# Kernel tuning notes

Hardware: AMD Instinct MI355X
Metric: run time of the kernel (lower is better)

Reference implementation:

```python
import jax, jax.numpy as jnp
import numpy as np

B, IN, OUT, D = 8192, 1024, 1024, 8


def setup_inputs() -> dict:
    key = jax.random.key(0)
    k1, k2, k3, k4 = jax.random.split(key, 4)
    # kaiming-uniform-ish init for weights, uniform for biases (values don't affect correctness)
    bound = 1.0 / np.sqrt(IN)
    return {
        "input": jax.random.normal(k1, (B, IN), dtype=jnp.float32),
        "w": jax.random.uniform(k2, (B, D), dtype=jnp.float32),
        "weights": jax.random.uniform(k3, (D, OUT, IN), dtype=jnp.float32, minval=-bound, maxval=bound),
        "biases": jax.random.uniform(k4, (D, OUT), dtype=jnp.float32, minval=-bound, maxval=bound),
    }


def reference(input, w, weights, biases):
    # Original math: weight[b] = sum_d w[b,d] * weights[d]  (shape [out,in])
    #                out[b]    = input[b] @ weight[b].T + sum_d w[b,d]*biases[d]
    # Restructured as one big GEMM + cheap dsize reduction:
    # tmp[b,d,o] = sum_i input[b,i] * weights[d,o,i]   (GEMM: [B,in] x [in, d*out])
    tmp = jnp.einsum('bi,doi->bdo', input, weights)
    out = jnp.einsum('bdo,bd->bo', tmp, w) + w @ biases
    return out
```

## Files before the change

### kernel.cpp

```cpp
#include <hip/hip_runtime.h>
#include <stdint.h>

typedef unsigned short u16;
typedef float v4f __attribute__((ext_vector_type(4)));
typedef short v8s __attribute__((ext_vector_type(8)));

#define B_   8192
#define IN_  1024
#define OUT_ 1024
#define D_   8

#define BM 128
#define BN 128
#define BK 64

__device__ __forceinline__ u16 f2bf(float f) {
  uint32_t u = __float_as_uint(f);
  u += 0x7fffu + ((u >> 16) & 1u);
  return (u16)(u >> 16);
}

__global__ __launch_bounds__(256) void convert_both(
    const float* __restrict__ input, const float* __restrict__ weights,
    u16* __restrict__ inBf, u16* __restrict__ wtBf) {
  int i4 = blockIdx.x * blockDim.x + threadIdx.x;
  const int n4 = (B_ * IN_) / 4;
  const float* src;
  u16* dst;
  int idx;
  if (i4 < n4) { src = input;   dst = inBf; idx = i4; }
  else         { src = weights; dst = wtBf; idx = i4 - n4; }
  float4 v = ((const float4*)src)[idx];
  ushort4 o;
  o.x = f2bf(v.x); o.y = f2bf(v.y); o.z = f2bf(v.z); o.w = f2bf(v.w);
  ((ushort4*)dst)[idx] = o;
}

__device__ __forceinline__ void gload_lds16(const u16* g, u16* l) {
  typedef __attribute__((address_space(1))) void gvoid;
  typedef __attribute__((address_space(3))) void lvoid;
  __builtin_amdgcn_global_load_lds((gvoid*)g, (lvoid*)l, 16, 0, 0);
}

__global__ __launch_bounds__(256, 2) void gemm_rs(
    const u16* __restrict__ A,
    const u16* __restrict__ Wt,
    const float* __restrict__ w,
    const float* __restrict__ biases,
    float* __restrict__ out) {
  __shared__ __align__(16) u16 As[2][BM * BK];
  __shared__ __align__(16) u16 Bs[3][BN * BK];

  const int id   = blockIdx.x;
  const int xcd  = id & 7;
  const int slot = id >> 3;
  const int by   = xcd + ((slot & 7) << 3);
  const int bx   = slot >> 3;

  const int tid  = threadIdx.x;
  const int wid  = tid >> 6;
  const int lane = tid & 63;
  const int wr   = wid >> 1, wc = wid & 1;
  const int quad = lane >> 4, l16 = lane & 15;
  const int m0   = by * BM;
  const int n0   = bx * BN;

  const int swz  = (lane & 7) ^ ((lane >> 3) & 7);
  const int rowS = wid * 32 + (lane >> 3);
  const u16* aBase[4];
  const u16* bBase[4];
  int cOff[4];
#pragma unroll
  for (int j = 0; j < 4; ++j) {
    const int row = rowS + j * 8;
    aBase[j] = A  + (size_t)(m0 + row) * IN_ + swz * 8;
    bBase[j] = Wt + (size_t)(n0 + row) * IN_ + swz * 8;
    cOff[j]  = (wid * 256 + j * 64 + lane) * 8;
  }

  const int aRow = wr * 64 + l16;
  const int bRow = wc * 64 + l16;
  const int e    = l16 & 7;
  int aCol[2];
#pragma unroll
  for (int h = 0; h < 2; ++h) aCol[h] = ((quad + 4 * h) ^ e) * 8;

  const v4f vzero = {0.f, 0.f, 0.f, 0.f};
  v4f acc[4][4];
#pragma unroll
  for (int mt = 0; mt < 4; ++mt)
#pragma unroll
    for (int nt = 0; nt < 4; ++nt) acc[mt][nt] = vzero;

  float wp[4][4];
#pragma unroll
  for (int mt = 0; mt < 4; ++mt)
#pragma unroll
    for (int r = 0; r < 4; ++r) {
      const int grow = m0 + wr * 64 + mt * 16 + quad * 4 + r;
      wp[mt][r] = fmaxf(w[(size_t)grow * D_], 1e-30f);
    }

  u16* aC_ = As[0];
  u16* aN  = As[1];
  u16* bC  = Bs[0];
  u16* bN  = Bs[1];
  u16* bS  = Bs[2];

#pragma unroll
  for (int j = 0; j < 4; ++j) gload_lds16(aBase[j], aC_ + cOff[j]);
#pragma unroll
  for (int j = 0; j < 4; ++j) gload_lds16(bBase[j], bC + cOff[j]);
#pragma unroll
  for (int j = 0; j < 4; ++j)
    gload_lds16(bBase[j] + (size_t)BK, bN + cOff[j]);
  asm volatile("s_waitcnt vmcnt(4) lgkmcnt(0)" ::: "memory");
  __builtin_amdgcn_s_barrier();

  for (int dd = 0; dd < D_; ++dd) {
    if (dd > 0) {
#pragma unroll
      for (int mt = 0; mt < 4; ++mt) {
#pragma unroll
        for (int r = 0; r < 4; ++r) {
          const int grow = m0 + wr * 64 + mt * 16 + quad * 4 + r;
          const float wn = fmaxf(w[(size_t)grow * D_ + dd], 1e-30f);
          const float ratio = wp[mt][r] / wn;
          wp[mt][r] = wn;
#pragma unroll
          for (int nt = 0; nt < 4; ++nt) acc[mt][nt][r] *= ratio;
        }
      }
    }
    for (int it = 0; it < 16; ++it) {
      const int t = dd * 16 + it;

      if (t < 127) {
        const int sit = (it + 1) & 15;
#pragma unroll
        for (int j = 0; j < 4; ++j)
          gload_lds16(aBase[j] + sit * BK, aN + cOff[j]);
      }
      if (t < 126) {
        const int it2  = it + 2;
        const int sdd2 = dd + (it2 >> 4);
        const int sit2 = it2 & 15;
#pragma unroll
        for (int j = 0; j < 4; ++j)
          gload_lds16(bBase[j] + (size_t)sdd2 * (OUT_ * IN_) + sit2 * BK,
                      bS + cOff[j]);
      }

      __builtin_amdgcn_s_setprio(1);
#pragma unroll
      for (int h = 0; h < 2; ++h) {
        v8s af[4], bf[4];
#pragma unroll
        for (int mt = 0; mt < 4; ++mt)
          af[mt] = *(const v8s*)(aC_ + (aRow + mt * 16) * BK + aCol[h]);
#pragma unroll
        for (int nt = 0; nt < 4; ++nt)
          bf[nt] = *(const v8s*)(bC + (bRow + nt * 16) * BK + aCol[h]);
#pragma unroll
        for (int mt = 0; mt < 4; ++mt)
#pragma unroll
          for (int nt = 0; nt < 4; ++nt)
            acc[mt][nt] = __builtin_amdgcn_mfma_f32_16x16x32_bf16(
                af[mt], bf[nt], acc[mt][nt], 0, 0, 0);
      }
      __builtin_amdgcn_s_setprio(0);

      if (t < 126) {
        asm volatile("s_waitcnt vmcnt(4)" ::: "memory");
        __builtin_amdgcn_s_barrier();
      } else if (t == 126) {
        asm volatile("s_waitcnt vmcnt(0)" ::: "memory");
        __builtin_amdgcn_s_barrier();
      }

      u16* ta = aC_; aC_ = aN; aN = ta;
      u16* tb = bC; bC = bN; bN = bS; bS = tb;
    }
  }

  float bcol[4][8];
#pragma unroll
  for (int nt = 0; nt < 4; ++nt) {
    const int col = n0 + wc * 64 + nt * 16 + l16;
#pragma unroll
    for (int dd = 0; dd < 8; ++dd) bcol[nt][dd] = biases[dd * OUT_ + col];
  }
#pragma unroll
  for (int mt = 0; mt < 4; ++mt) {
#pragma unroll
    for (int r = 0; r < 4; ++r) {
      const int grow = m0 + wr * 64 + mt * 16 + quad * 4 + r;
      const v4f* wpg = (const v4f*)(w + (size_t)grow * D_);
      const v4f wa = wpg[0], wb = wpg[1];
      const float wlast = wp[mt][r];
#pragma unroll
      for (int nt = 0; nt < 4; ++nt) {
        const int col = n0 + wc * 64 + nt * 16 + l16;
        const float bias = wa[0] * bcol[nt][0] + wa[1] * bcol[nt][1] +
                           wa[2] * bcol[nt][2] + wa[3] * bcol[nt][3] +
                           wb[0] * bcol[nt][4] + wb[1] * bcol[nt][5] +
                           wb[2] * bcol[nt][6] + wb[3] * bcol[nt][7];
        out[(size_t)grow * OUT_ + col] = acc[mt][nt][r] * wlast + bias;
      }
    }
  }
}

extern "C" void kernel_launch(void* const* d_in, const int* in_sizes, int n_in,
                              void* d_out, int out_size, void* d_ws, size_t ws_size,
                              hipStream_t stream) {
  const float* input   = (const float*)d_in[0];
  const float* w       = (const float*)d_in[1];
  const float* weights = (const float*)d_in[2];
  const float* biases  = (const float*)d_in[3];
  float* out = (float*)d_out;

  u16* inBf = (u16*)d_ws;
  u16* wtBf = inBf + (size_t)B_ * IN_;

  const int totalF4 = (B_ * IN_ + D_ * OUT_ * IN_) / 4;
  convert_both<<<dim3(totalF4 / 256), 256, 0, stream>>>(input, weights, inBf, wtBf);
  gemm_rs<<<dim3(512), 256, 0, stream>>>(inBf, wtBf, w, biases, out);
}
```

Before: 236.1 us.

## Use 256x128 tiles with 8 waves and a split-phase interleaved LDS pipeline

```diff
diff --git a/kernel.cpp b/kernel.cpp
--- a/kernel.cpp
+++ b/kernel.cpp
@@ -10,7 +10,7 @@
 #define OUT_ 1024
 #define D_   8
 
-#define BM 128
+#define BM 256
 #define BN 128
 #define BK 64
 
@@ -42,20 +42,20 @@
   __builtin_amdgcn_global_load_lds((gvoid*)g, (lvoid*)l, 16, 0, 0);
 }
 
-__global__ __launch_bounds__(256, 2) void gemm_rs(
+__global__ __launch_bounds__(512, 2) void gemm_8w(
     const u16* __restrict__ A,
     const u16* __restrict__ Wt,
     const float* __restrict__ w,
     const float* __restrict__ biases,
     float* __restrict__ out) {
   __shared__ __align__(16) u16 As[2][BM * BK];
-  __shared__ __align__(16) u16 Bs[3][BN * BK];
+  __shared__ __align__(16) u16 Bs[4][BN * BK];
 
   const int id   = blockIdx.x;
   const int xcd  = id & 7;
   const int slot = id >> 3;
-  const int by   = xcd + ((slot & 7) << 3);
-  const int bx   = slot >> 3;
+  const int by   = xcd + ((slot & 3) << 3);
+  const int bx   = slot >> 2;
 
   const int tid  = threadIdx.x;
   const int wid  = tid >> 6;
@@ -65,17 +65,20 @@
   const int m0   = by * BM;
   const int n0   = bx * BN;
 
-  const int swz  = (lane & 7) ^ ((lane >> 3) & 7);
-  const int rowS = wid * 32 + (lane >> 3);
+  const int swz  = (tid & 7) ^ ((tid >> 3) & 7);
+  const int rowT = tid >> 3;
   const u16* aBase[4];
-  const u16* bBase[4];
-  int cOff[4];
+  const u16* bBase[2];
+  int aOff[4], bOff[2];
 #pragma unroll
   for (int j = 0; j < 4; ++j) {
-    const int row = rowS + j * 8;
-    aBase[j] = A  + (size_t)(m0 + row) * IN_ + swz * 8;
-    bBase[j] = Wt + (size_t)(n0 + row) * IN_ + swz * 8;
-    cOff[j]  = (wid * 256 + j * 64 + lane) * 8;
+    aBase[j] = A + (size_t)(m0 + j * 64 + rowT) * IN_ + swz * 8;
+    aOff[j]  = (j * 512 + tid) * 8;
+  }
+#pragma unroll
+  for (int j = 0; j < 2; ++j) {
+    bBase[j] = Wt + (size_t)(n0 + j * 64 + rowT) * IN_ + swz * 8;
+    bOff[j]  = (j * 512 + tid) * 8;
   }
 
   const int aRow = wr * 64 + l16;
@@ -101,20 +104,14 @@
       wp[mt][r] = fmaxf(w[(size_t)grow * D_], 1e-30f);
     }
 
-  u16* aC_ = As[0];
-  u16* aN  = As[1];
-  u16* bC  = Bs[0];
-  u16* bN  = Bs[1];
-  u16* bS  = Bs[2];
-
-#pragma unroll
-  for (int j = 0; j < 4; ++j) gload_lds16(aBase[j], aC_ + cOff[j]);
-#pragma unroll
-  for (int j = 0; j < 4; ++j) gload_lds16(bBase[j], bC + cOff[j]);
-#pragma unroll
-  for (int j = 0; j < 4; ++j)
-    gload_lds16(bBase[j] + (size_t)BK, bN + cOff[j]);
-  asm volatile("s_waitcnt vmcnt(4) lgkmcnt(0)" ::: "memory");
+#pragma unroll
+  for (int j = 0; j < 4; ++j) gload_lds16(aBase[j], &As[0][aOff[j]]);
+#pragma unroll
+  for (int j = 0; j < 2; ++j) gload_lds16(bBase[j], &Bs[0][bOff[j]]);
+#pragma unroll
+  for (int j = 0; j < 2; ++j)
+    gload_lds16(bBase[j] + (size_t)BK, &Bs[1][bOff[j]]);
+  asm volatile("s_waitcnt vmcnt(2) lgkmcnt(0)" ::: "memory");
   __builtin_amdgcn_s_barrier();
 
   for (int dd = 0; dd < D_; ++dd) {
@@ -132,54 +129,70 @@
         }
       }
     }
-    for (int it = 0; it < 16; ++it) {
-      const int t = dd * 16 + it;
-
-      if (t < 127) {
+    for (int ip = 0; ip < 4; ++ip) {
+#pragma unroll
+      for (int u = 0; u < 4; ++u) {
+        const int it  = ip * 4 + u;
+        const int kA  = u & 1;
+        const int kAn = kA ^ 1;
+        const int kB  = u;
+        const int kBs = (u + 2) & 3;
         const int sit = (it + 1) & 15;
-#pragma unroll
-        for (int j = 0; j < 4; ++j)
-          gload_lds16(aBase[j] + sit * BK, aN + cOff[j]);
+        const int su  = dd * 16 + it + 2;
+        const size_t bo = (size_t)((su >> 4) & 7) * (OUT_ * IN_) +
+                          (size_t)(su & 15) * BK;
+
+        {
+          v8s af[4], bf[4];
+#pragma unroll
+          for (int mt = 0; mt < 4; ++mt)
+            af[mt] = *(const v8s*)(&As[kA][(aRow + mt * 16) * BK + aCol[0]]);
+#pragma unroll
+          for (int nt = 0; nt < 4; ++nt)
+            bf[nt] = *(const v8s*)(&Bs[kB][(bRow + nt * 16) * BK + aCol[0]]);
+          gload_lds16(aBase[0] + sit * BK, &As[kAn][aOff[0]]);
+          gload_lds16(aBase[1] + sit * BK, &As[kAn][aOff[1]]);
+          __builtin_amdgcn_s_barrier();
+          asm volatile("s_waitcnt lgkmcnt(0)" ::: "memory");
+          __builtin_amdgcn_sched_barrier(0);
+          __builtin_amdgcn_s_setprio(1);
+#pragma unroll
+          for (int mt = 0; mt < 4; ++mt)
+#pragma unroll
+            for (int nt = 0; nt < 4; ++nt)
+              acc[mt][nt] = __builtin_amdgcn_mfma_f32_16x16x32_bf16(
+                  af[mt], bf[nt], acc[mt][nt], 0, 0, 0);
+          __builtin_amdgcn_s_setprio(0);
+          __builtin_amdgcn_s_barrier();
+        }
+
+        {
+          v8s af[4], bf[4];
+#pragma unroll
+          for (int mt = 0; mt < 4; ++mt)
+            af[mt] = *(const v8s*)(&As[kA][(aRow + mt * 16) * BK + aCol[1]]);
+#pragma unroll
+          for (int nt = 0; nt < 4; ++nt)
+            bf[nt] = *(const v8s*)(&Bs[kB][(bRow + nt * 16) * BK + aCol[1]]);
+          gload_lds16(aBase[2] + sit * BK, &As[kAn][aOff[2]]);
+          gload_lds16(aBase[3] + sit * BK, &As[kAn][aOff[3]]);
+          gload_lds16(bBase[0] + bo, &Bs[kBs][bOff[0]]);
+          gload_lds16(bBase[1] + bo, &Bs[kBs][bOff[1]]);
+          __builtin_amdgcn_s_barrier();
+          asm volatile("s_waitcnt lgkmcnt(0)" ::: "memory");
+          __builtin_amdgcn_sched_barrier(0);
+          __builtin_amdgcn_s_setprio(1);
+#pragma unroll
+          for (int mt = 0; mt < 4; ++mt)
+#pragma unroll
+            for (int nt = 0; nt < 4; ++nt)
+              acc[mt][nt] = __builtin_amdgcn_mfma_f32_16x16x32_bf16(
+                  af[mt], bf[nt], acc[mt][nt], 0, 0, 0);
+          __builtin_amdgcn_s_setprio(0);
+          asm volatile("s_waitcnt vmcnt(2)" ::: "memory");
+          __builtin_amdgcn_s_barrier();
+        }
       }
-      if (t < 126) {
-        const int it2  = it + 2;
-        const int sdd2 = dd + (it2 >> 4);
-        const int sit2 = it2 & 15;
-#pragma unroll
-        for (int j = 0; j < 4; ++j)
-          gload_lds16(bBase[j] + (size_t)sdd2 * (OUT_ * IN_) + sit2 * BK,
-                      bS + cOff[j]);
-      }
-
-      __builtin_amdgcn_s_setprio(1);
-#pragma unroll
-      for (int h = 0; h < 2; ++h) {
-        v8s af[4], bf[4];
-#pragma unroll
-        for (int mt = 0; mt < 4; ++mt)
-          af[mt] = *(const v8s*)(aC_ + (aRow + mt * 16) * BK + aCol[h]);
-#pragma unroll
-        for (int nt = 0; nt < 4; ++nt)
-          bf[nt] = *(const v8s*)(bC + (bRow + nt * 16) * BK + aCol[h]);
-#pragma unroll
-        for (int mt = 0; mt < 4; ++mt)
-#pragma unroll
-          for (int nt = 0; nt < 4; ++nt)
-            acc[mt][nt] = __builtin_amdgcn_mfma_f32_16x16x32_bf16(
-                af[mt], bf[nt], acc[mt][nt], 0, 0, 0);
-      }
-      __builtin_amdgcn_s_setprio(0);
-
-      if (t < 126) {
-        asm volatile("s_waitcnt vmcnt(4)" ::: "memory");
-        __builtin_amdgcn_s_barrier();
-      } else if (t == 126) {
-        asm volatile("s_waitcnt vmcnt(0)" ::: "memory");
-        __builtin_amdgcn_s_barrier();
-      }
-
-      u16* ta = aC_; aC_ = aN; aN = ta;
-      u16* tb = bC; bC = bN; bN = bS; bS = tb;
     }
   }
 
@@ -225,5 +238,5 @@
 
   const int totalF4 = (B_ * IN_ + D_ * OUT_ * IN_) / 4;
   convert_both<<<dim3(totalF4 / 256), 256, 0, stream>>>(input, weights, inBf, wtBf);
-  gemm_rs<<<dim3(512), 256, 0, stream>>>(inBf, wtBf, w, biases, out);
-}
+  gemm_8w<<<dim3(256), 512, 0, stream>>>(inBf, wtBf, w, biases, out);
+}
```

Measured after the change: 243.3 us. 3.1% more time.
